# Optimization experiments

Hardware: AMD Instinct MI355X
Metric: run time of the kernel (lower is better)

## Reference

```python
import jax, jax.numpy as jnp
import numpy as np

B, S, D = 4, 2048, 1024
NH, NKV = 16, 4
HD = D // NH  # 64


def _rope(x, freqs):
    # x: [B, H, S, HD], freqs: [B, S, HD//2]
    cos = jnp.concatenate([jnp.cos(freqs), jnp.cos(freqs)], axis=-1)[:, None]  # [B,1,S,HD]
    sin = jnp.concatenate([jnp.sin(freqs), jnp.sin(freqs)], axis=-1)[:, None]
    x1, x2 = x[..., : HD // 2], x[..., HD // 2:]
    rot = jnp.concatenate([-x2, x1], axis=-1)
    return x * cos + rot * sin


def setup_inputs() -> dict:
    key = jax.random.key(0)
    ks = jax.random.split(key, 9)
    return {
        "hidden_states": jax.random.normal(ks[0], (B, S, D), jnp.float32),
        "rotary_pos_emb": jax.random.normal(ks[1], (B, S, HD // 2), jnp.float32),
        "Wq": jax.random.normal(ks[2], (D, NH * HD), jnp.float32) * 0.02,
        "bq": jax.random.normal(ks[3], (NH * HD,), jnp.float32) * 0.02,
        "Wk": jax.random.normal(ks[4], (D, NKV * HD), jnp.float32) * 0.02,
        "bk": jax.random.normal(ks[5], (NKV * HD,), jnp.float32) * 0.02,
        "Wv": jax.random.normal(ks[6], (D, NKV * HD), jnp.float32) * 0.02,
        "bv": jax.random.normal(ks[7], (NKV * HD,), jnp.float32) * 0.02,
        "Wo": jax.random.normal(ks[8], (NH * HD, D), jnp.float32) * 0.02,
    }


def reference(hidden_states, rotary_pos_emb, Wq, bq, Wk, bk, Wv, bv, Wo):
    b, s, _ = hidden_states.shape
    # projections -> [B, H, S, HD]
    q = (hidden_states @ Wq + bq).reshape(b, s, NH, HD).transpose(0, 2, 1, 3)
    k = (hidden_states @ Wk + bk).reshape(b, s, NKV, HD).transpose(0, 2, 1, 3)
    v = (hidden_states @ Wv + bv).reshape(b, s, NKV, HD).transpose(0, 2, 1, 3)
    q = _rope(q, rotary_pos_emb)
    k = _rope(k, rotary_pos_emb)
    groups = NH // NKV
    k = jnp.repeat(k, groups, axis=1)  # [B, NH, S, HD]
    v = jnp.repeat(v, groups, axis=1)
    scaling = HD ** -0.5
    scores = jnp.einsum("bhqd,bhkd->bhqk", q, k) * scaling
    probs = jax.nn.softmax(scores.astype(jnp.float32), axis=-1).astype(q.dtype)
    out = jnp.einsum("bhqk,bhkd->bhqd", probs, v)
    out = out.transpose(0, 2, 1, 3).reshape(b, s, NH * HD)
    return out @ Wo
```

## Files before the change

### kernel.cpp

```cpp
#include <hip/hip_runtime.h>
#include <hip/hip_bf16.h>

#define BB 4
#define SS 2048
#define DD 1024
#define NH 16
#define NKV 4
#define HD 64
#define MROWS (BB*SS)
#define NQKV (NH*HD + 2*NKV*HD)
#define KOFF (NH*HD)

typedef short v8s __attribute__((ext_vector_type(8)));
typedef short v4s __attribute__((ext_vector_type(4)));
typedef float v4f __attribute__((ext_vector_type(4)));
typedef unsigned short u16;
typedef unsigned int u32;

__device__ __forceinline__ float bf2f(u16 u){
  union { float f; u32 i; } x; x.i = ((u32)u) << 16; return x.f;
}
__device__ __forceinline__ u16 f2bf(float f){
  union { __hip_bfloat16 h; u16 u; } x; x.h = __float2bfloat16(f); return x.u;
}
__device__ __forceinline__ u32 cvtpk(float lo, float hi){
  u32 r;
  asm("v_cvt_pk_bf16_f32 %0, %1, %2" : "=v"(r) : "v"(lo), "v"(hi));
  return r;
}
__device__ __forceinline__ float fmax3(float a, float b, float c){
  return fmaxf(fmaxf(a, b), c);
}
__device__ __forceinline__ void gl_lds16(const u16* g, u16* l){
  __builtin_amdgcn_global_load_lds(
      (const __attribute__((address_space(1))) u32*)g,
      (__attribute__((address_space(3))) u32*)l, 16, 0, 0);
}


__global__ void cast_x(const float* __restrict__ in, u16* __restrict__ out, int n4){
  int i = blockIdx.x*256 + threadIdx.x;
  if (i >= n4) return;
  float4 v = reinterpret_cast<const float4*>(in)[i];
  ushort4 o;
  o.x = f2bf(v.x); o.y = f2bf(v.y); o.z = f2bf(v.z); o.w = f2bf(v.w);
  reinterpret_cast<ushort4*>(out)[i] = o;
}

__global__ void build_bqkv(const float* __restrict__ Wq, const float* __restrict__ Wk,
                           const float* __restrict__ Wv, const float* __restrict__ bq,
                           const float* __restrict__ bk, const float* __restrict__ bv,
                           u16* __restrict__ Bt, float* __restrict__ bias){
  int idx = blockIdx.x*256 + threadIdx.x;
  int n = idx >> 10, k = idx & 1023;
  float v;
  if (n < 1024)      v = Wq[k*1024 + n];
  else if (n < 1280) v = Wk[k*256 + (n-1024)];
  else               v = Wv[k*256 + (n-1280)];
  Bt[idx] = f2bf(v);
  if (k == 0) bias[n] = (n < 1024) ? bq[n] : (n < 1280 ? bk[n-1024] : bv[n-1280]);
}

__global__ void build_wo(const float* __restrict__ Wo, u16* __restrict__ Bt){
  int idx = blockIdx.x*256 + threadIdx.x;
  int n = idx >> 10, k = idx & 1023;
  Bt[idx] = f2bf(Wo[k*1024 + n]);
}

__global__ void rope_k(u16* __restrict__ QKV, const float* __restrict__ fr){
  int idx = blockIdx.x*256 + threadIdx.x;
  int d  = idx & 31;
  int hh = (idx >> 5) & 3;
  long row = idx >> 7;
  int col = KOFF + hh*HD + d;
  u16* p = QKV + row*NQKV;
  float x1 = bf2f(p[col]);
  float x2 = bf2f(p[col+32]);
  float f = fr[row*32 + d];
  float sn, cs; __sincosf(f, &sn, &cs);
  p[col]    = f2bf(x1*cs - x2*sn);
  p[col+32] = f2bf(x2*cs + x1*sn);
}


template<bool BIAS, typename OT>
__global__ __launch_bounds__(256) void gemm_bt(
    const u16* __restrict__ A, const u16* __restrict__ Bt,
    const float* __restrict__ bias, OT* __restrict__ C,
    int K, int ldc)
{
  __shared__ u16 As[128*64];
  __shared__ u16 Bs[128*64];
  const int tid = threadIdx.x;
  const int wid = tid >> 6, lane = tid & 63;
  const int g = lane >> 4, c = lane & 15;
  const long brow = (long)blockIdx.y * 128;
  const long bcol = (long)blockIdx.x * 128;
  const int wr = (wid >> 1) * 64, wc = (wid & 1) * 64;
  const int srow = tid >> 3;
  const int scol = (tid & 7) * 8;
  const u16* ga = &A [(brow + srow)*K + scol];
  const u16* gb = &Bt[(bcol + srow)*K + scol];
  u16* la = &As[(wid*8)*64];
  u16* lb = &Bs[(wid*8)*64];
  v4f acc[4][4] = {};
  for (int kt = 0; kt < K; kt += 64) {
    __syncthreads();
    #pragma unroll
    for (int e = 0; e < 4; ++e) {
      gl_lds16(ga + (long)e*32*K + kt, la + e*32*64);
      gl_lds16(gb + (long)e*32*K + kt, lb + e*32*64);
    }
    __syncthreads();
    #pragma unroll
    for (int ks = 0; ks < 2; ++ks) {
      v8s af[4], bf[4];
      #pragma unroll
      for (int m=0;m<4;m++) af[m] = *reinterpret_cast<const v8s*>(&As[(wr + m*16 + c)*64 + ks*32 + g*8]);
      #pragma unroll
      for (int n=0;n<4;n++) bf[n] = *reinterpret_cast<const v8s*>(&Bs[(wc + n*16 + c)*64 + ks*32 + g*8]);
      __builtin_amdgcn_s_setprio(1);
      #pragma unroll
      for (int m=0;m<4;m++)
        #pragma unroll
        for (int n=0;n<4;n++)
          acc[m][n] = __builtin_amdgcn_mfma_f32_16x16x32_bf16(af[m], bf[n], acc[m][n], 0,0,0);
      __builtin_amdgcn_s_setprio(0);
    }
  }
  #pragma unroll
  for (int m=0;m<4;m++)
    #pragma unroll
    for (int n=0;n<4;n++) {
      int col = (int)bcol + wc + n*16 + c;
      float badd = BIAS ? bias[col] : 0.0f;
      #pragma unroll
      for (int r2=0;r2<4;r2++){
        long row = brow + wr + m*16 + g*4 + r2;
        float v = acc[m][n][r2] + badd;
        if constexpr (sizeof(OT)==2) C[row*ldc + col] = (OT)f2bf(v);
        else                         C[row*ldc + col] = (OT)v;
      }
    }
}


__global__ __launch_bounds__(512) void attn_k(const u16* __restrict__ QKV,
                                              const float* __restrict__ fr,
                                              u16* __restrict__ Out){
  __shared__ u16 Ks[2][64][72];
  __shared__ u16 Vs[2][64][72];
  const int tid = threadIdx.x;
  const int wid = tid >> 6, lane = tid & 63;
  const int g = lane >> 4, c = lane & 15;
  const int qt = blockIdx.x & 7;
  const int bh = blockIdx.x >> 3;
  const int b = bh >> 4, h = bh & 15;
  const int kvh = h >> 2;
  const u16* Qb = QKV + (long)b*SS*NQKV + h*HD;
  const u16* Kb = QKV + (long)b*SS*NQKV + KOFF + kvh*HD;
  const u16* Vb = Kb + NKV*HD;

  const float SCL = 0.125f * 1.44269504088896f;
  v8s qf[2][2];
  #pragma unroll
  for (int qn=0;qn<2;qn++){
    int lrow = qt*256 + wid*32 + qn*16 + c;
    v8s q0 = *reinterpret_cast<const v8s*>(&Qb[(long)lrow*NQKV + g*8]);
    v8s q1 = *reinterpret_cast<const v8s*>(&Qb[(long)lrow*NQKV + 32 + g*8]);
    const float* frp = fr + ((long)b*SS + lrow)*32 + g*8;
    float4 f0 = *reinterpret_cast<const float4*>(frp);
    float4 f1 = *reinterpret_cast<const float4*>(frp + 4);
    float fa[8] = {f0.x,f0.y,f0.z,f0.w,f1.x,f1.y,f1.z,f1.w};
    float r0[8], r1[8];
    #pragma unroll
    for (int j=0;j<8;j++){
      float x1 = bf2f((u16)q0[j]), x2 = bf2f((u16)q1[j]);
      float sn, cs; __sincosf(fa[j], &sn, &cs);
      r0[j] = (x1*cs - x2*sn) * SCL;
      r1[j] = (x2*cs + x1*sn) * SCL;
    }
    union { v8s v; u32 w[4]; } a0, a1;
    #pragma unroll
    for (int wi=0;wi<4;wi++){
      a0.w[wi] = cvtpk(r0[2*wi], r0[2*wi+1]);
      a1.w[wi] = cvtpk(r1[2*wi], r1[2*wi+1]);
    }
    qf[qn][0] = a0.v; qf[qn][1] = a1.v;
  }

  v8s onesf;
  {
    short ov = (c==0) ? (short)0x3F80 : (short)0;
    #pragma unroll
    for (int j=0;j<8;j++) onesf[j] = ov;
  }

  v4f o[2][5] = {};
  float mr[2] = {0.f, 0.f};

  const int krow = tid >> 3;
  const int kcol = (tid & 7) * 8;
  const int key0 = 2*(tid >> 4);
  const int dg4  = (tid & 15) * 4;
  const int slot0 = 32*(key0>>5) + 8*((key0>>2)&3) + 4*((key0>>4)&1) + (key0&3);
  int vofs[4];
  #pragma unroll
  for (int j=0;j<4;j++){
    int d = dg4 + j;
    int idx = (((slot0>>3) ^ (d>>3)) << 3) | (slot0 & 7);
    vofs[j] = d*72 + idx;
  }
  u16* VsF = &Vs[0][0][0];

  const u16* kp  = Kb + (long)krow*NQKV + kcol;
  const u16* vp0 = Vb + (long)key0*NQKV + dg4;
  const u16* vp1 = vp0 + NQKV;

  v8s kreg;
  union { v4s v; u32 w[2]; } vr0, vr1;

  {
    kreg  = *reinterpret_cast<const v8s*>(kp);
    vr0.v = *reinterpret_cast<const v4s*>(vp0);
    vr1.v = *reinterpret_cast<const v4s*>(vp1);
    *reinterpret_cast<v8s*>(&Ks[0][krow][kcol]) = kreg;
    #pragma unroll
    for (int j=0;j<4;j++){
      u32 pkd = __builtin_amdgcn_perm(vr1.w[j>>1], vr0.w[j>>1],
                                      (j&1) ? 0x07060302u : 0x05040100u);
      *reinterpret_cast<u32*>(&VsF[vofs[j]]) = pkd;
    }
  }
  __syncthreads();

  int p = 0;
  for (int t = 0; t < SS/64; ++t){
    if (t+1 < SS/64) {
      long off = (long)(t+1)*64*NQKV;
      kreg  = *reinterpret_cast<const v8s*>(kp  + off);
      vr0.v = *reinterpret_cast<const v4s*>(vp0 + off);
      vr1.v = *reinterpret_cast<const v4s*>(vp1 + off);
    }

    v4f st[4][2];
    #pragma unroll
    for (int qn=0;qn<2;qn++){
      v4f mi = {-mr[qn], -mr[qn], -mr[qn], -mr[qn]};
      #pragma unroll
      for (int km=0;km<4;km++) st[km][qn] = mi;
    }
    #pragma unroll
    for (int ks=0;ks<2;ks++){
      v8s kf[4];
      #pragma unroll
      for (int km=0;km<4;km++)
        kf[km] = *reinterpret_cast<const v8s*>(&Ks[p][km*16 + c][ks*32 + g*8]);
      __builtin_amdgcn_s_setprio(1);
      #pragma unroll
      for (int km=0;km<4;km++)
        #pragma unroll
        for (int qn=0;qn<2;qn++)
          st[km][qn] = __builtin_amdgcn_mfma_f32_16x16x32_bf16(kf[km], qf[qn][ks], st[km][qn], 0,0,0);
      __builtin_amdgcn_s_setprio(0);
    }

    float al[2];
    bool upd[2];
    #pragma unroll
    for (int qn=0;qn<2;qn++){
      float t0 = fmax3(st[0][qn][0], st[0][qn][1], st[0][qn][2]);
      float t1 = fmax3(st[0][qn][3], st[1][qn][0], st[1][qn][1]);
      float t2 = fmax3(st[1][qn][2], st[1][qn][3], st[2][qn][0]);
      float t3 = fmax3(st[2][qn][1], st[2][qn][2], st[2][qn][3]);
      float t4 = fmax3(st[3][qn][0], st[3][qn][1], st[3][qn][2]);
      float mx = fmaxf(fmax3(t0, t1, t2), fmax3(t3, t4, st[3][qn][3]));
      upd[qn] = !__all(mx <= 8.0f);
      al[qn] = 1.0f;
      if (upd[qn]) {
        mx = fmaxf(mx, __shfl_xor(mx, 16));
        mx = fmaxf(mx, __shfl_xor(mx, 32));
        float d = fmaxf(mx, 0.0f);
        al[qn] = __builtin_amdgcn_exp2f(-d);
        mr[qn] += d;
        #pragma unroll
        for (int km=0;km<4;km++)
          #pragma unroll
          for (int r2=0;r2<4;r2++)
            st[km][qn][r2] -= d;
      }
      #pragma unroll
      for (int km=0;km<4;km++)
        #pragma unroll
        for (int r2=0;r2<4;r2++)
          st[km][qn][r2] = __builtin_amdgcn_exp2f(st[km][qn][r2]);
    }

    v8s pa[2][2];
    #pragma unroll
    for (int qm=0;qm<2;qm++)
      #pragma unroll
      for (int ks=0;ks<2;ks++){
        union { v8s v; u32 w[4]; } u;
        u.w[0] = cvtpk(st[2*ks  ][qm][0], st[2*ks  ][qm][1]);
        u.w[1] = cvtpk(st[2*ks  ][qm][2], st[2*ks  ][qm][3]);
        u.w[2] = cvtpk(st[2*ks+1][qm][0], st[2*ks+1][qm][1]);
        u.w[3] = cvtpk(st[2*ks+1][qm][2], st[2*ks+1][qm][3]);
        pa[qm][ks] = u.v;
      }

    if (upd[0] | upd[1]) {
      #pragma unroll
      for (int qm=0;qm<2;qm++)
        #pragma unroll
        for (int r2=0;r2<4;r2++){
          float a = __shfl(al[qm], g*4 + r2);
          #pragma unroll
          for (int dn=0;dn<5;dn++) o[qm][dn][r2] *= a;
        }
    }

    #pragma unroll
    for (int ks=0;ks<2;ks++){
      __builtin_amdgcn_s_setprio(1);
      #pragma unroll
      for (int dn=0;dn<4;dn++){
        int d0 = dn*16 + c;
        v8s vf = *reinterpret_cast<const v8s*>(&Vs[p][d0][(((ks*4+g) ^ (d0>>3)) << 3)]);
        #pragma unroll
        for (int qm=0;qm<2;qm++)
          o[qm][dn] = __builtin_amdgcn_mfma_f32_16x16x32_bf16(pa[qm][ks], vf, o[qm][dn], 0,0,0);
      }
      #pragma unroll
      for (int qm=0;qm<2;qm++)
        o[qm][4] = __builtin_amdgcn_mfma_f32_16x16x32_bf16(pa[qm][ks], onesf, o[qm][4], 0,0,0);
      __builtin_amdgcn_s_setprio(0);
    }

    if (t+1 < SS/64) {
      *reinterpret_cast<v8s*>(&Ks[p^1][krow][kcol]) = kreg;
      const int bofs = (p^1) * (64*72);
      #pragma unroll
      for (int j=0;j<4;j++){
        u32 pkd = __builtin_amdgcn_perm(vr1.w[j>>1], vr0.w[j>>1],
                                        (j&1) ? 0x07060302u : 0x05040100u);
        *reinterpret_cast<u32*>(&VsF[bofs + vofs[j]]) = pkd;
      }
    }
    __syncthreads();
    p ^= 1;
  }

  #pragma unroll
  for (int qm=0;qm<2;qm++)
    #pragma unroll
    for (int r2=0;r2<4;r2++){
      float l = __shfl(o[qm][4][r2], lane & 48);
      float inv = 1.0f / l;
      long row = (long)b*SS + qt*256 + wid*32 + qm*16 + g*4 + r2;
      #pragma unroll
      for (int dn=0;dn<4;dn++)
        Out[row*DD + h*HD + dn*16 + c] = f2bf(o[qm][dn][r2] * inv);
    }
}


extern "C" void kernel_launch(void* const* d_in, const int* in_sizes, int n_in,
                              void* d_out, int out_size, void* d_ws, size_t ws_size,
                              hipStream_t stream)
{
  const float* hs = (const float*)d_in[0];
  const float* fr = (const float*)d_in[1];
  const float* Wq = (const float*)d_in[2];
  const float* bq = (const float*)d_in[3];
  const float* Wk = (const float*)d_in[4];
  const float* bk = (const float*)d_in[5];
  const float* Wv = (const float*)d_in[6];
  const float* bv = (const float*)d_in[7];
  const float* Wo = (const float*)d_in[8];
  float* out = (float*)d_out;
  char* ws = (char*)d_ws;

  u16*   Xb   = (u16*)(ws);
  u16*   Bqkv = (u16*)(ws + 16777216);
  u16*   WoT  = (u16*)(ws + 16777216 + 3145728);
  float* bias = (float*)(ws + 16777216 + 3145728 + 2097152);
  u16*   QKV  = (u16*)(ws + 22028288);
  u16*   AO   = (u16*)(ws + 22028288 + 25165824);

  cast_x   <<<8192, 256, 0, stream>>>(hs, Xb, MROWS*DD/4);
  build_bqkv<<<6144, 256, 0, stream>>>(Wq, Wk, Wv, bq, bk, bv, Bqkv, bias);
  build_wo <<<4096, 256, 0, stream>>>(Wo, WoT);
  gemm_bt<true,  u16>  <<<dim3(NQKV/128, MROWS/128), 256, 0, stream>>>(Xb, Bqkv, bias, QKV, DD, NQKV);
  rope_k   <<<MROWS*NKV*32/256, 256, 0, stream>>>(QKV, fr);
  attn_k   <<<BB*NH*(SS/256), 512, 0, stream>>>(QKV, fr, AO);
  gemm_bt<false, float><<<dim3(DD/128, MROWS/128), 256, 0, stream>>>(AO, WoT, nullptr, out, DD, DD);
}
```

Before: 177.4 us.

## Halve GEMM K-tile to 32 and precompute RoPE sin/cos table for attention

The shared GEMM kernel now stages a 32-wide K slice per iteration instead of 64. This halves LDS use and may allow more blocks per CU, but it doubles the number of barrier pairs per K loop and removes the inner two-step unroll. Separately, a new kernel precomputes cos/sin pairs into a table (reusing the Bqkv weight buffer after the QKV GEMM), so the attention kernel loads them instead of calling sincos per Q element. This costs an extra launch and about 2 MB of extra memory traffic.

```diff
diff --git a/kernel.cpp b/kernel.cpp
--- a/kernel.cpp
+++ b/kernel.cpp
@@ -65,6 +65,13 @@
   int idx = blockIdx.x*256 + threadIdx.x;
   int n = idx >> 10, k = idx & 1023;
   Bt[idx] = f2bf(Wo[k*1024 + n]);
+}
+
+__global__ void build_trig(const float* __restrict__ fr, float2* __restrict__ trig){
+  int i = blockIdx.x*256 + threadIdx.x;
+  float f = fr[i];
+  float sn, cs; __sincosf(f, &sn, &cs);
+  trig[i] = make_float2(cs, sn);
 }
 
 __global__ void rope_k(u16* __restrict__ QKV, const float* __restrict__ fr){
@@ -89,44 +96,40 @@
     const float* __restrict__ bias, OT* __restrict__ C,
     int K, int ldc)
 {
-  __shared__ u16 As[128*64];
-  __shared__ u16 Bs[128*64];
+  __shared__ u16 As[128*32];
+  __shared__ u16 Bs[128*32];
   const int tid = threadIdx.x;
   const int wid = tid >> 6, lane = tid & 63;
   const int g = lane >> 4, c = lane & 15;
   const long brow = (long)blockIdx.y * 128;
   const long bcol = (long)blockIdx.x * 128;
   const int wr = (wid >> 1) * 64, wc = (wid & 1) * 64;
-  const int srow = tid >> 3;
-  const int scol = (tid & 7) * 8;
+  const int srow = tid >> 2;
+  const int scol = (tid & 3) * 8;
   const u16* ga = &A [(brow + srow)*K + scol];
   const u16* gb = &Bt[(bcol + srow)*K + scol];
-  u16* la = &As[(wid*8)*64];
-  u16* lb = &Bs[(wid*8)*64];
+  u16* la = &As[(wid*64)*8];
+  u16* lb = &Bs[(wid*64)*8];
   v4f acc[4][4] = {};
-  for (int kt = 0; kt < K; kt += 64) {
+  for (int kt = 0; kt < K; kt += 32) {
     __syncthreads();
-    #pragma unroll
-    for (int e = 0; e < 4; ++e) {
-      gl_lds16(ga + (long)e*32*K + kt, la + e*32*64);
-      gl_lds16(gb + (long)e*32*K + kt, lb + e*32*64);
-    }
+    gl_lds16(ga + kt,          la);
+    gl_lds16(ga + 64*K + kt,   la + 256*8);
+    gl_lds16(gb + kt,          lb);
+    gl_lds16(gb + 64*K + kt,   lb + 256*8);
     __syncthreads();
-    #pragma unroll
-    for (int ks = 0; ks < 2; ++ks) {
-      v8s af[4], bf[4];
-      #pragma unroll
-      for (int m=0;m<4;m++) af[m] = *reinterpret_cast<const v8s*>(&As[(wr + m*16 + c)*64 + ks*32 + g*8]);
-      #pragma unroll
-      for (int n=0;n<4;n++) bf[n] = *reinterpret_cast<const v8s*>(&Bs[(wc + n*16 + c)*64 + ks*32 + g*8]);
-      __builtin_amdgcn_s_setprio(1);
-      #pragma unroll
-      for (int m=0;m<4;m++)
-        #pragma unroll
-        for (int n=0;n<4;n++)
-          acc[m][n] = __builtin_amdgcn_mfma_f32_16x16x32_bf16(af[m], bf[n], acc[m][n], 0,0,0);
-      __builtin_amdgcn_s_setprio(0);
-    }
+    v8s af[4], bf[4];
+    #pragma unroll
+    for (int m=0;m<4;m++) af[m] = *reinterpret_cast<const v8s*>(&As[(wr + m*16 + c)*32 + g*8]);
+    #pragma unroll
+    for (int n=0;n<4;n++) bf[n] = *reinterpret_cast<const v8s*>(&Bs[(wc + n*16 + c)*32 + g*8]);
+    __builtin_amdgcn_s_setprio(1);
+    #pragma unroll
+    for (int m=0;m<4;m++)
+      #pragma unroll
+      for (int n=0;n<4;n++)
+        acc[m][n] = __builtin_amdgcn_mfma_f32_16x16x32_bf16(af[m], bf[n], acc[m][n], 0,0,0);
+    __builtin_amdgcn_s_setprio(0);
   }
   #pragma unroll
   for (int m=0;m<4;m++)
@@ -146,7 +149,7 @@
 
 
 __global__ __launch_bounds__(512) void attn_k(const u16* __restrict__ QKV,
-                                              const float* __restrict__ fr,
+                                              const float2* __restrict__ trig,
                                               u16* __restrict__ Out){
   __shared__ u16 Ks[2][64][72];
   __shared__ u16 Vs[2][64][72];
@@ -168,17 +171,17 @@
     int lrow = qt*256 + wid*32 + qn*16 + c;
     v8s q0 = *reinterpret_cast<const v8s*>(&Qb[(long)lrow*NQKV + g*8]);
     v8s q1 = *reinterpret_cast<const v8s*>(&Qb[(long)lrow*NQKV + 32 + g*8]);
-    const float* frp = fr + ((long)b*SS + lrow)*32 + g*8;
-    float4 f0 = *reinterpret_cast<const float4*>(frp);
-    float4 f1 = *reinterpret_cast<const float4*>(frp + 4);
-    float fa[8] = {f0.x,f0.y,f0.z,f0.w,f1.x,f1.y,f1.z,f1.w};
+    const float4* tp = reinterpret_cast<const float4*>(
+        trig + ((long)b*SS + lrow)*32 + g*8);
+    float4 t0 = tp[0], t1 = tp[1], t2 = tp[2], t3 = tp[3];
+    float cs_[8] = {t0.x,t0.z,t1.x,t1.z,t2.x,t2.z,t3.x,t3.z};
+    float sn_[8] = {t0.y,t0.w,t1.y,t1.w,t2.y,t2.w,t3.y,t3.w};
     float r0[8], r1[8];
     #pragma unroll
     for (int j=0;j<8;j++){
       float x1 = bf2f((u16)q0[j]), x2 = bf2f((u16)q1[j]);
-      float sn, cs; __sincosf(fa[j], &sn, &cs);
-      r0[j] = (x1*cs - x2*sn) * SCL;
-      r1[j] = (x2*cs + x1*sn) * SCL;
+      r0[j] = (x1*cs_[j] - x2*sn_[j]) * SCL;
+      r1[j] = (x2*cs_[j] + x1*sn_[j]) * SCL;
     }
     union { v8s v; u32 w[4]; } a0, a1;
     #pragma unroll
@@ -387,12 +390,14 @@
   float* bias = (float*)(ws + 16777216 + 3145728 + 2097152);
   u16*   QKV  = (u16*)(ws + 22028288);
   u16*   AO   = (u16*)(ws + 22028288 + 25165824);
-
-  cast_x   <<<8192, 256, 0, stream>>>(hs, Xb, MROWS*DD/4);
+  float2* trig = (float2*)Bqkv;
+
+  cast_x    <<<8192, 256, 0, stream>>>(hs, Xb, MROWS*DD/4);
   build_bqkv<<<6144, 256, 0, stream>>>(Wq, Wk, Wv, bq, bk, bv, Bqkv, bias);
-  build_wo <<<4096, 256, 0, stream>>>(Wo, WoT);
+  build_wo  <<<4096, 256, 0, stream>>>(Wo, WoT);
   gemm_bt<true,  u16>  <<<dim3(NQKV/128, MROWS/128), 256, 0, stream>>>(Xb, Bqkv, bias, QKV, DD, NQKV);
-  rope_k   <<<MROWS*NKV*32/256, 256, 0, stream>>>(QKV, fr);
-  attn_k   <<<BB*NH*(SS/256), 512, 0, stream>>>(QKV, fr, AO);
+  build_trig<<<1024, 256, 0, stream>>>(fr, trig);
+  rope_k    <<<MROWS*NKV*32/256, 256, 0, stream>>>(QKV, fr);
+  attn_k    <<<BB*NH*(SS/256), 512, 0, stream>>>(QKV, trig, AO);
   gemm_bt<false, float><<<dim3(DD/128, MROWS/128), 256, 0, stream>>>(AO, WoT, nullptr, out, DD, DD);
 }
```

Result: no change. 180.2 us (+1.6%).
